# Optimization experiments

Measured on AMD Instinct MI355X. Metric: run time of the kernel, lower is better.

The kernel has to match this reference:

```python
import jax, jax.numpy as jnp
import numpy as np
import math

H, KVH, DH = 8, 1, 256
CAP = 50.0
THETA = 10000.0
HIDDEN = [2048, 1024, 1024]


def _rope_cos_sin(pos, dh=DH, theta=THETA):
    # pos: [b, s] int -> cos/sin: [b, s, dh] (Gemma style: freqs duplicated)
    inv_freq = 1.0 / (theta ** (jnp.arange(0, dh, 2, dtype=jnp.float32) / dh))
    freqs = pos.astype(jnp.float32)[..., None] * inv_freq  # [b, s, dh/2]
    emb = jnp.concatenate([freqs, freqs], axis=-1)
    return jnp.cos(emb), jnp.sin(emb)


def _rotate_half(x):
    x1, x2 = jnp.split(x, 2, axis=-1)
    return jnp.concatenate([-x2, x1], axis=-1)


def _apply_rope(q, k, cos, sin):
    # q: [b,H,s,d], k: [b,KVH,s,d]; cos/sin: [b,s,d] -> broadcast over heads
    c = cos[:, None].astype(q.dtype)
    s = sin[:, None].astype(q.dtype)
    return q * c + _rotate_half(q) * s, k * c + _rotate_half(k) * s


def setup_inputs() -> dict:
    key = jax.random.key(0)
    ks = jax.random.split(key, 32)
    inp = {
        'hs0': jax.random.normal(ks[0], (8, 968, 2048), jnp.float32),
        'hs1': jax.random.normal(ks[1], (8, 6, 1024), jnp.float32),
        'hs2': jax.random.normal(ks[2], (8, 50, 1024), jnp.float32),
        'attention_mask': jnp.zeros((8, 1, 1024, 1024), jnp.float32),
        'pos0': jnp.sort(jax.random.randint(ks[3], (8, 968), 0, 1024), axis=-1),
        'pos1': jnp.sort(jax.random.randint(ks[4], (8, 6), 0, 1024), axis=-1),
        'pos2': jnp.sort(jax.random.randint(ks[5], (8, 50), 0, 1024), axis=-1),
    }
    ki = 6
    for b, hid in enumerate(HIDDEN):
        inp[f'wq{b}'] = 0.02 * jax.random.normal(ks[ki + 0], (hid, H * DH), jnp.float32)
        inp[f'wk{b}'] = 0.02 * jax.random.normal(ks[ki + 1], (hid, KVH * DH), jnp.float32)
        inp[f'wv{b}'] = 0.02 * jax.random.normal(ks[ki + 2], (hid, KVH * DH), jnp.float32)
        inp[f'wo{b}'] = 0.02 * jax.random.normal(ks[ki + 3], (H * DH, hid), jnp.float32)
        ki += 4
    return inp


def _joint_attn(hs_all, pos_all, mask, wq, wk, wv, wo):
    b = hs_all[0].shape[0]
    q_lens = [h.shape[1] for h in hs_all]
    qs, kss, vs = [], [], []
    for hs, pos, Wq, Wk, Wv in zip(hs_all, pos_all, wq, wk, wv):
        s = hs.shape[1]
        q = (hs @ Wq).reshape(b, s, H, DH).transpose(0, 2, 1, 3)
        k = (hs @ Wk).reshape(b, s, KVH, DH).transpose(0, 2, 1, 3)
        v = (hs @ Wv).reshape(b, s, KVH, DH).transpose(0, 2, 1, 3)
        cos, sin = _rope_cos_sin(pos)
        q, k = _apply_rope(q, k, cos, sin)
        # repeat_kv: MQA -> expand KV heads to H
        qs.append(q)
        kss.append(jnp.repeat(k, H // KVH, axis=1))
        vs.append(jnp.repeat(v, H // KVH, axis=1))
    q = jnp.concatenate(qs, axis=2)   # [b,H,S,d]
    k = jnp.concatenate(kss, axis=2)
    v = jnp.concatenate(vs, axis=2)
    scores = jnp.einsum('bhqd,bhkd->bhqk', q, k) / math.sqrt(DH)
    scores = jnp.tanh(scores / CAP) * CAP + mask  # tanh soft-capping
    p = jax.nn.softmax(scores.astype(jnp.float32), axis=-1).astype(q.dtype)
    out = jnp.einsum('bhqk,bhkd->bhqd', p, v)     # [b,H,S,d]
    out = out.transpose(0, 2, 1, 3).reshape(b, sum(q_lens), H * DH)
    outs, off = [], 0
    for ql, Wo in zip(q_lens, wo):
        outs.append(out[:, off:off + ql] @ Wo)
        off += ql
    return tuple(outs)


def reference(hs0, hs1, hs2, attention_mask, pos0, pos1, pos2,
              wq0, wk0, wv0, wo0, wq1, wk1, wv1, wo1, wq2, wk2, wv2, wo2):
    return _joint_attn((hs0, hs1, hs2), (pos0, pos1, pos2), attention_mask,
                       (wq0, wq1, wq2), (wk0, wk1, wk2), (wv0, wv1, wv2),
                       (wo0, wo1, wo2))
```

## Files before the change

### kernel.cpp

```cpp
#include <hip/hip_runtime.h>
#include <hip/hip_bf16.h>
#include <math.h>

namespace {
constexpr int Bn = 8, Sn = 1024, Hn = 8, DHn = 256, HDn = 2048;
constexpr size_t QB0 = 0;
constexpr size_t QB1 = (size_t)20 * 64 * 4096;
constexpr size_t QB2 = QB1 + (size_t)20 * 32 * 4096;
constexpr size_t HB0 = 0;
constexpr size_t HB1 = (size_t)61 * 64 * 4096;
constexpr size_t HB2 = HB1 + (size_t)1 * 32 * 4096;
constexpr size_t OB0 = 0;
constexpr size_t OB1 = (size_t)16 * 64 * 4096;
constexpr size_t OB2 = OB1 + (size_t)8 * 64 * 4096;
}

using bf16x8 = __attribute__((ext_vector_type(8))) short;
using f32x4  = __attribute__((ext_vector_type(4))) float;
using i32x4  = __attribute__((ext_vector_type(4))) int;

__device__ __forceinline__ float bf2f(unsigned short u) {
  unsigned int x = ((unsigned int)u) << 16;
  return __builtin_bit_cast(float, x);
}
__device__ __forceinline__ unsigned short f2bf(float f) {
  unsigned int x = __builtin_bit_cast(unsigned int, f);
  x += 0x7fff + ((x >> 16) & 1);
  return (unsigned short)(x >> 16);
}
__device__ __forceinline__ bf16x8 pack8(const float4& u, const float4& v) {
  bf16x8 r;
  r[0] = (short)f2bf(u.x); r[1] = (short)f2bf(u.y); r[2] = (short)f2bf(u.z); r[3] = (short)f2bf(u.w);
  r[4] = (short)f2bf(v.x); r[5] = (short)f2bf(v.y); r[6] = (short)f2bf(v.z); r[7] = (short)f2bf(v.w);
  return r;
}
__device__ __forceinline__ void gload_lds16(const void* g, void* l) {
  __builtin_amdgcn_global_load_lds(
      (const __attribute__((address_space(1))) void*)g,
      (__attribute__((address_space(3))) void*)l, 16, 0, 0);
}
__device__ __forceinline__ unsigned cvtpk(float lo, float hi) {
  unsigned r;
  asm("v_cvt_pk_bf16_f32 %0, %1, %2" : "=v"(r) : "v"(lo), "v"(hi));
  return r;
}

__device__ __forceinline__ void convW_body(
    const float* __restrict__ W, unsigned short* __restrict__ dstBase,
    int K, int N, int nb, int kb, float (*S)[132], int t)
{
  const int kl = t >> 5, nq = (t & 31) * 4;
  for (int kk = kl; kk < 64; kk += 8) {
    const float4 v = *(const float4*)(W + (size_t)(kb * 64 + kk) * N + nb * 128 + nq);
    S[kk][nq] = v.x; S[kk][nq + 1] = v.y; S[kk][nq + 2] = v.z; S[kk][nq + 3] = v.w;
  }
  __syncthreads();
  unsigned short* chunk = dstBase + ((size_t)nb * (K >> 5) + kb * 2) * 4096;
#pragma unroll
  for (int j = 0; j < 4; ++j) {
    const int q = t * 4 + j;
    const int r = q >> 3, g = q & 7;
    bf16x8 o;
#pragma unroll
    for (int e = 0; e < 8; ++e) o[e] = (short)f2bf(S[g * 8 + e][r]);
    *(bf16x8*)(chunk + (g >> 2) * 4096 + r * 32 + (((g & 3) ^ ((r >> 1) & 3)) * 8)) = o;
  }
}

__global__ __launch_bounds__(256) void convAll(
    const float* __restrict__ wq0, const float* __restrict__ wk0, const float* __restrict__ wv0,
    const float* __restrict__ wq1, const float* __restrict__ wk1, const float* __restrict__ wv1,
    const float* __restrict__ wq2, const float* __restrict__ wk2, const float* __restrict__ wv2,
    const float* __restrict__ hs0, const float* __restrict__ hs1, const float* __restrict__ hs2,
    unsigned short* __restrict__ qkvT, unsigned short* __restrict__ hsT)
{
  __shared__ float S[64][132];
  const int bid = blockIdx.x;
  const int t = threadIdx.x;

  if (bid < 1280) {
    const float* W; unsigned short* dst; int K, N, nb, kb;
    if (bid < 512)       { W = wq0; dst = qkvT + QB0;                  K = 2048; N = 2048; nb = bid & 15; kb = bid >> 4; }
    else if (bid < 576)  { int r = bid - 512;  W = wk0; dst = qkvT + QB0 + (size_t)16 * 64 * 4096; K = 2048; N = 256; nb = r & 1; kb = r >> 1; }
    else if (bid < 640)  { int r = bid - 576;  W = wv0; dst = qkvT + QB0 + (size_t)18 * 64 * 4096; K = 2048; N = 256; nb = r & 1; kb = r >> 1; }
    else if (bid < 896)  { int r = bid - 640;  W = wq1; dst = qkvT + QB1;                  K = 1024; N = 2048; nb = r & 15; kb = r >> 4; }
    else if (bid < 928)  { int r = bid - 896;  W = wk1; dst = qkvT + QB1 + (size_t)16 * 32 * 4096; K = 1024; N = 256; nb = r & 1; kb = r >> 1; }
    else if (bid < 960)  { int r = bid - 928;  W = wv1; dst = qkvT + QB1 + (size_t)18 * 32 * 4096; K = 1024; N = 256; nb = r & 1; kb = r >> 1; }
    else if (bid < 1216) { int r = bid - 960;  W = wq2; dst = qkvT + QB2;                  K = 1024; N = 2048; nb = r & 15; kb = r >> 4; }
    else if (bid < 1248) { int r = bid - 1216; W = wk2; dst = qkvT + QB2 + (size_t)16 * 32 * 4096; K = 1024; N = 256; nb = r & 1; kb = r >> 1; }
    else                 { int r = bid - 1248; W = wv2; dst = qkvT + QB2 + (size_t)18 * 32 * 4096; K = 1024; N = 256; nb = r & 1; kb = r >> 1; }
    convW_body(W, dst, K, N, nb, kb, S, t);
  } else {
    const float* A; unsigned short* dst; int K, M_total, mb, kb;
    if (bid < 3232)      { int it = bid - 1280; A = hs0; dst = hsT + HB0; K = 2048; M_total = 7744; mb = it >> 5; kb = it & 31; }
    else if (bid < 3248) { int it = bid - 3232; A = hs1; dst = hsT + HB1; K = 1024; M_total = 48;   mb = 0;       kb = it; }
    else                 { int it = bid - 3248; A = hs2; dst = hsT + HB2; K = 1024; M_total = 400;  mb = it >> 4; kb = it & 15; }
    unsigned short* chunk = dst + ((size_t)mb * (K >> 5) + kb * 2) * 4096;
#pragma unroll
    for (int j = 0; j < 4; ++j) {
      const int q = j * 256 + t;
      const int r = q >> 3, g = q & 7;
      int m = mb * 128 + r;
      if (m >= M_total) m = mb * 128;
      const float* src = A + (size_t)m * K + kb * 64 + g * 8;
      const float4 u = *(const float4*)(src);
      const float4 v = *(const float4*)(src + 4);
      *(bf16x8*)(chunk + (g >> 2) * 4096 + r * 32 + (((g & 3) ^ ((r >> 1) & 3)) * 8)) = pack8(u, v);
    }
  }
}

__global__ __launch_bounds__(256) void convWo(
    const float* __restrict__ wo0, const float* __restrict__ wo1, const float* __restrict__ wo2,
    unsigned short* __restrict__ woT)
{
  __shared__ float S[64][132];
  const int bid = blockIdx.x;
  const float* W; unsigned short* dst; int N, nb, kb;
  if (bid < 512)      { W = wo0; dst = woT + OB0; N = 2048; nb = bid & 15; kb = bid >> 4; }
  else if (bid < 768) { int r = bid - 512; W = wo1; dst = woT + OB1; N = 1024; nb = r & 7; kb = r >> 3; }
  else                { int r = bid - 768; W = wo2; dst = woT + OB2; N = 1024; nb = r & 7; kb = r >> 3; }
  convW_body(W, dst, HDn, N, nb, kb, S, threadIdx.x);
}

__global__ __launch_bounds__(256) void gemm_qkv(
    const unsigned short* __restrict__ hsT, const unsigned short* __restrict__ qkvT,
    unsigned short* __restrict__ Qh, unsigned short* __restrict__ Kh,
    unsigned short* __restrict__ Vt)
{
  __shared__ __align__(16) short As[2][4096];
  __shared__ __align__(16) short Bs[2][4096];
  const int tid = threadIdx.x;
  const int w  = tid >> 6, l = tid & 63;
  const int wm = w >> 1,  wn = w & 1;
  const int lc = l & 15,  lg = l >> 4;

  const int bid = blockIdx.x;
  int bx, by, L, K, c_off, M_total;
  const unsigned short *aBase, *wBase;
  if (bid < 1220)      { bx = bid % 20; by = bid / 20; L = 968; K = 2048; c_off = 0;   M_total = 7744; aBase = hsT + HB0; wBase = qkvT + QB0; }
  else if (bid < 1240) { bx = bid - 1220; by = 0;      L = 6;   K = 1024; c_off = 968; M_total = 48;   aBase = hsT + HB1; wBase = qkvT + QB1; }
  else                 { int r = bid - 1240; bx = r % 20; by = r / 20; L = 50; K = 1024; c_off = 974; M_total = 400; aBase = hsT + HB2; wBase = qkvT + QB2; }
  const int kcN = K >> 5;
  const int bm0 = by * 128;

  int region, nbL, cb0;
  if (bx < 16)      { region = 0; nbL = bx;      cb0 = bx * 128; }
  else if (bx < 18) { region = 1; nbL = bx - 16; cb0 = (bx - 16) * 128; }
  else              { region = 2; nbL = bx - 18; cb0 = (bx - 18) * 128; }
  const unsigned short* WTr = wBase +
      (region == 0 ? (size_t)0 : (region == 1 ? (size_t)16 * kcN * 4096
                                              : (size_t)18 * kcN * 4096));
  const char* bChunk0 = (const char*)(WTr + (size_t)nbL * kcN * 4096);
  const char* aChunk0 = (const char*)(aBase + (size_t)by * kcN * 4096);

  f32x4 acc[4][4];
#pragma unroll
  for (int i = 0; i < 4; ++i)
#pragma unroll
    for (int j = 0; j < 4; ++j) acc[i][j] = (f32x4){0.f, 0.f, 0.f, 0.f};

  auto issue = [&](int kc, int nb) {
    const char* sa = aChunk0 + (size_t)kc * 8192;
    const char* sb = bChunk0 + (size_t)kc * 8192;
    char* da = (char*)&As[nb][0];
    char* db = (char*)&Bs[nb][0];
    gload_lds16(sa + tid * 16, da + tid * 16);
    gload_lds16(sa + tid * 16 + 4096, da + tid * 16 + 4096);
    gload_lds16(sb + tid * 16, db + tid * 16);
    gload_lds16(sb + tid * 16 + 4096, db + tid * 16 + 4096);
  };

  issue(0, 0);
  for (int kt = 0; kt < kcN; ++kt) {
    const int cur = kt & 1;
    __builtin_amdgcn_s_barrier();
    if (kt + 1 < kcN) {
      issue(kt + 1, cur ^ 1);
      asm volatile("s_waitcnt vmcnt(4)" ::: "memory");
    } else {
      asm volatile("s_waitcnt vmcnt(0)" ::: "memory");
    }
    __builtin_amdgcn_s_barrier();
    __builtin_amdgcn_sched_barrier(0);
    bf16x8 af[4], bfg[4];
#pragma unroll
    for (int mi = 0; mi < 4; ++mi) {
      const int row = wm * 64 + mi * 16 + lc;
      af[mi] = *(const bf16x8*)((const char*)&As[cur][0] + row * 64 +
                                ((lg ^ ((row >> 1) & 3)) * 16));
    }
#pragma unroll
    for (int ni = 0; ni < 4; ++ni) {
      const int row = wn * 64 + ni * 16 + lc;
      bfg[ni] = *(const bf16x8*)((const char*)&Bs[cur][0] + row * 64 +
                                 ((lg ^ ((row >> 1) & 3)) * 16));
    }
#pragma unroll
    for (int mi = 0; mi < 4; ++mi)
#pragma unroll
      for (int ni = 0; ni < 4; ++ni)
        acc[mi][ni] = __builtin_amdgcn_mfma_f32_16x16x32_bf16(af[mi], bfg[ni], acc[mi][ni], 0, 0, 0);
  }

#pragma unroll
  for (int mi = 0; mi < 4; ++mi) {
    const int gm = bm0 + wm * 64 + mi * 16 + lg * 4;
#pragma unroll
    for (int r = 0; r < 4; ++r) {
      const int m = gm + r;
      if (m < M_total) {
        const int cb = m / L, cs = m - cb * L;
#pragma unroll
        for (int ni = 0; ni < 4; ++ni) {
          const int colL = cb0 + wn * 64 + ni * 16 + lc;
          const unsigned short v = f2bf(acc[mi][ni][r]);
          if (region == 0) {
            const int hh = colL >> 8, dd = colL & 255;
            Qh[(((size_t)cb * Hn + hh) * Sn + c_off + cs) * DHn + dd] = v;
          } else if (region == 1) {
            Kh[((size_t)cb * Sn + c_off + cs) * DHn + colL] = v;
          } else {
            Vt[((size_t)cb * DHn + colL) * Sn + c_off + cs] = v;
          }
        }
      }
    }
  }
}

__global__ __launch_bounds__(256) void gemm_wo(
    const unsigned short* __restrict__ A, const unsigned short* __restrict__ woT,
    float* __restrict__ C)
{
  __shared__ __align__(16) short As[2][4096];
  __shared__ __align__(16) short Bs[2][4096];
  const int tid = threadIdx.x;
  const int w  = tid >> 6, l = tid & 63;
  const int wm = w >> 1,  wn = w & 1;
  const int lc = l & 15,  lg = l >> 4;

  const int bid = blockIdx.x;
  int bx, by, L, N, a_off, M_total;
  const unsigned short* wb;
  float* Cg;
  if (bid < 976)      { bx = bid & 15; by = bid >> 4; L = 968; N = 2048; a_off = 0;   M_total = 7744; wb = woT + OB0; Cg = C; }
  else if (bid < 984) { bx = bid - 976; by = 0;       L = 6;   N = 1024; a_off = 968; M_total = 48;   wb = woT + OB1; Cg = C + (size_t)7744 * 2048; }
  else                { int r = bid - 984; bx = r & 7; by = r >> 3; L = 50; N = 1024; a_off = 974; M_total = 400; wb = woT + OB2; Cg = C + (size_t)7744 * 2048 + (size_t)48 * 1024; }
  const int bm0 = by * 128;
  const char* chunk0 = (const char*)(wb + (size_t)bx * 64 * 4096);

  const int gcont = (tid & 3) ^ ((tid >> 3) & 3);
  const char* aRow[2];
#pragma unroll
  for (int j = 0; j < 2; ++j) {
    int m = bm0 + (tid >> 2) + j * 64;
    if (m >= M_total) m = 0;
    const int cb = m / L, cs = m - cb * L;
    aRow[j] = (const char*)(A + (size_t)(cb * Sn + a_off + cs) * HDn) + gcont * 16;
  }

  f32x4 acc[4][4];
#pragma unroll
  for (int i = 0; i < 4; ++i)
#pragma unroll
    for (int j = 0; j < 4; ++j) acc[i][j] = (f32x4){0.f, 0.f, 0.f, 0.f};

  auto issue = [&](int kc, int nb) {
    char* da = (char*)&As[nb][0];
    char* db = (char*)&Bs[nb][0];
    gload_lds16(aRow[0] + (size_t)kc * 64, da + tid * 16);
    gload_lds16(aRow[1] + (size_t)kc * 64, da + tid * 16 + 4096);
    const char* sb = chunk0 + (size_t)kc * 8192;
    gload_lds16(sb + tid * 16, db + tid * 16);
    gload_lds16(sb + tid * 16 + 4096, db + tid * 16 + 4096);
  };

  issue(0, 0);
  for (int kt = 0; kt < 64; ++kt) {
    const int cur = kt & 1;
    __builtin_amdgcn_s_barrier();
    if (kt + 1 < 64) {
      issue(kt + 1, cur ^ 1);
      asm volatile("s_waitcnt vmcnt(4)" ::: "memory");
    } else {
      asm volatile("s_waitcnt vmcnt(0)" ::: "memory");
    }
    __builtin_amdgcn_s_barrier();
    __builtin_amdgcn_sched_barrier(0);
    bf16x8 af[4], bfg[4];
#pragma unroll
    for (int mi = 0; mi < 4; ++mi) {
      const int row = wm * 64 + mi * 16 + lc;
      af[mi] = *(const bf16x8*)((const char*)&As[cur][0] + row * 64 +
                                ((lg ^ ((row >> 1) & 3)) * 16));
    }
#pragma unroll
    for (int ni = 0; ni < 4; ++ni) {
      const int row = wn * 64 + ni * 16 + lc;
      bfg[ni] = *(const bf16x8*)((const char*)&Bs[cur][0] + row * 64 +
                                 ((lg ^ ((row >> 1) & 3)) * 16));
    }
#pragma unroll
    for (int mi = 0; mi < 4; ++mi)
#pragma unroll
      for (int ni = 0; ni < 4; ++ni)
        acc[mi][ni] = __builtin_amdgcn_mfma_f32_16x16x32_bf16(af[mi], bfg[ni], acc[mi][ni], 0, 0, 0);
  }

#pragma unroll
  for (int mi = 0; mi < 4; ++mi) {
    const int gm = bm0 + wm * 64 + mi * 16 + lg * 4;
#pragma unroll
    for (int r = 0; r < 4; ++r) {
      const int m = gm + r;
      if (m < M_total) {
        const int cb = m / L, cs = m - cb * L;
#pragma unroll
        for (int ni = 0; ni < 4; ++ni) {
          const int col = bx * 128 + wn * 64 + ni * 16 + lc;
          Cg[(size_t)(cb * L + cs) * N + col] = acc[mi][ni][r];
        }
      }
    }
  }
}

__global__ __launch_bounds__(128) void rope_k(
    unsigned short* __restrict__ Kh,
    const int* __restrict__ p0, const int* __restrict__ p1, const int* __restrict__ p2)
{
  const int t = blockIdx.x, b = t >> 10, s = t & 1023;
  int p;
  if (s < 968)      p = p0[b * 968 + s];
  else if (s < 974) p = p1[b * 6 + (s - 968)];
  else              p = p2[b * 50 + (s - 974)];
  const float pf = (float)p;
  const float c0 = -0.07195578415606394f;
  const int d = threadIdx.x;
  const float inv = __expf(c0 * (float)d);
  float cs, sn;
  sincosf(pf * inv, &sn, &cs);
  unsigned short* base = Kh + ((size_t)b * Sn + s) * DHn;
  const float x1 = bf2f(base[d]), x2 = bf2f(base[d + 128]);
  base[d]       = f2bf(x1 * cs - x2 * sn);
  base[d + 128] = f2bf(x2 * cs + x1 * sn);
}

__global__ __launch_bounds__(512) void attn_mfma(
    const unsigned short* __restrict__ Qh, const unsigned short* __restrict__ Kh,
    const unsigned short* __restrict__ Vt, const float* __restrict__ mask,
    const int* __restrict__ p0, const int* __restrict__ p1, const int* __restrict__ p2,
    unsigned short* __restrict__ O)
{
  __shared__ __align__(16) short KsB[2][8192];
  __shared__ __align__(16) short VsB[2][8192];
  __shared__ __align__(16) float Ms[2][512];
  const int tid = threadIdx.x;
  const int w  = tid >> 6;
  const int l  = tid & 63;
  const int lc = l & 15;
  const int lg = l >> 4;
  const int bid = blockIdx.x;
  const int b  = bid & 7;
  const int q0 = (bid >> 3) * 16;
  const int srow = q0 + lc;

  const char* KgB = (const char*)(Kh + (size_t)b * Sn * DHn);
  const char* VgB = (const char*)(Vt + (size_t)b * DHn * Sn);

  auto stage = [&](int kt, int nb) {
    const char* kg = KgB + (size_t)kt * 16384;
    const char* vg = VgB + (size_t)kt * 64;
#pragma unroll
    for (int j = 0; j < 2; ++j) {
      const int chunk = w * 2 + j;
      const int o = chunk * 1024 + l * 16;
      const int srcK = o ^ (((o >> 9) & 7) << 4);
      gload_lds16(kg + srcK, (char*)&KsB[nb][0] + chunk * 1024);
    }
#pragma unroll
    for (int j = 0; j < 2; ++j) {
      const int chunk = w * 2 + j;
      const int o = chunk * 1024 + l * 16;
      const int x = o ^ (((o >> 7) & 3) << 4);
      gload_lds16(vg + (size_t)(x >> 6) * 2048 + (x & 63),
                  (char*)&VsB[nb][0] + chunk * 1024);
    }
    if (l < 16) {
      const int q = 2 * w + (l >> 3);
      const int kb = (((l & 7) * 4) - 4 * q) & 31;
      const float* mg = mask + ((size_t)b * Sn + q0 + q) * Sn + kt * 32 + kb;
      gload_lds16(mg, (char*)&Ms[nb][0] + w * 256);
    }
  };

  stage(0, 0);

  int p;
  if (srow < 968)      p = p0[b * 968 + srow];
  else if (srow < 974) p = p1[b * 6 + (srow - 968)];
  else                 p = p2[b * 50 + (srow - 974)];
  const float pf = (float)p;
  const float c0 = -0.07195578415606394f;

  const unsigned short* qrow = Qh + (((size_t)b * Hn + w) * Sn + srow) * DHn;
  bf16x8 qf[8];
#pragma unroll
  for (int dt = 0; dt < 8; ++dt)
    qf[dt] = *(const bf16x8*)(qrow + dt * 32 + lg * 8);
#pragma unroll
  for (int dt = 0; dt < 4; ++dt) {
#pragma unroll
    for (int j = 0; j < 8; ++j) {
      const int d = dt * 32 + lg * 8 + j;
      const float inv = __expf(c0 * (float)d);
      float cs, sn;
      sincosf(pf * inv, &sn, &cs);
      const float x1 = bf2f((unsigned short)qf[dt][j]);
      const float x2 = bf2f((unsigned short)qf[dt + 4][j]);
      qf[dt][j]     = (short)f2bf(x1 * cs - x2 * sn);
      qf[dt + 4][j] = (short)f2bf(x2 * cs + x1 * sn);
    }
  }

  f32x4 accO[16];
#pragma unroll
  for (int i = 0; i < 16; ++i) accO[i] = (f32x4){0.f, 0.f, 0.f, 0.f};
  float lsum = 0.f;

  const float C1 = 3.6067376022e-3f;
  const float RC = -144.26950408889634f;
  const float L2E = 1.4426950408889634f;

  const int mo0 = lc * 128 + (((lg * 4) + 4 * lc) & 31) * 4;
  const int mo1 = lc * 128 + (((16 + lg * 4) + 4 * lc) & 31) * 4;
  const int sidx0 = (((lg & 1) * 2) * 16 + lc) * 4;
  const int sidx1 = sidx0 + 64;
  const bool hiT = (lg >= 2);

  int cur = 0;
  for (int kt = 0; kt < 32; ++kt) {
    if (kt + 1 < 32) {
      stage(kt + 1, cur ^ 1);
      asm volatile("s_waitcnt vmcnt(5)" ::: "memory");
    } else {
      asm volatile("s_waitcnt vmcnt(0)" ::: "memory");
    }
    __builtin_amdgcn_s_barrier();
    __builtin_amdgcn_sched_barrier(0);

    const char* Ks = (const char*)&KsB[cur][0];
    const char* Vs = (const char*)&VsB[cur][0];
    const char* Mw = (const char*)&Ms[cur][0];

    const float4 mv0 = *(const float4*)(Mw + mo0);
    const float4 mv1 = *(const float4*)(Mw + mo1);

    f32x4 sc[2];
    __builtin_amdgcn_s_setprio(1);
#pragma unroll
    for (int ct = 0; ct < 2; ++ct) {
      f32x4 a0 = (f32x4){0.f, 0.f, 0.f, 0.f};
      f32x4 a1 = (f32x4){0.f, 0.f, 0.f, 0.f};
      const int row = ct * 16 + lc;
      const int sw = (row & 7) << 4;
#pragma unroll
      for (int dt = 0; dt < 8; dt += 2) {
        const int byt0 = (row * 512 + dt * 64 + lg * 16) ^ sw;
        const int byt1 = (row * 512 + (dt + 1) * 64 + lg * 16) ^ sw;
        const bf16x8 kf0 = *(const bf16x8*)(Ks + byt0);
        const bf16x8 kf1 = *(const bf16x8*)(Ks + byt1);
        a0 = __builtin_amdgcn_mfma_f32_16x16x32_bf16(kf0, qf[dt], a0, 0, 0, 0);
        a1 = __builtin_amdgcn_mfma_f32_16x16x32_bf16(kf1, qf[dt + 1], a1, 0, 0, 0);
      }
      sc[ct] = a0 + a1;
    }
    __builtin_amdgcn_s_setprio(0);

    const float mA[8] = {mv0.x, mv0.y, mv0.z, mv0.w, mv1.x, mv1.y, mv1.z, mv1.w};
    float pr[8];
#pragma unroll
    for (int t = 0; t < 2; ++t) {
#pragma unroll
      for (int r = 0; r < 4; ++r) {
        const float e2 = __builtin_amdgcn_exp2f(sc[t][r] * C1);
        const float rr = __builtin_amdgcn_rcpf(e2 + 1.f);
        const float pv = __builtin_amdgcn_exp2f(fmaf(rr, RC, mA[t * 4 + r] * L2E));
        lsum += pv;
        pr[t * 4 + r] = pv;
      }
    }

    const int t0w0 = (int)cvtpk(pr[0], pr[1]);
    const int t0w1 = (int)cvtpk(pr[2], pr[3]);
    const int t1w0 = (int)cvtpk(pr[4], pr[5]);
    const int t1w1 = (int)cvtpk(pr[6], pr[7]);
    const int b00 = __builtin_amdgcn_ds_bpermute(sidx0, t0w0);
    const int b01 = __builtin_amdgcn_ds_bpermute(sidx0, t0w1);
    const int b02 = __builtin_amdgcn_ds_bpermute(sidx1, t0w0);
    const int b03 = __builtin_amdgcn_ds_bpermute(sidx1, t0w1);
    const int b10 = __builtin_amdgcn_ds_bpermute(sidx0, t1w0);
    const int b11 = __builtin_amdgcn_ds_bpermute(sidx0, t1w1);
    const int b12 = __builtin_amdgcn_ds_bpermute(sidx1, t1w0);
    const int b13 = __builtin_amdgcn_ds_bpermute(sidx1, t1w1);
    i32x4 pd;
    pd[0] = hiT ? b10 : b00;
    pd[1] = hiT ? b11 : b01;
    pd[2] = hiT ? b12 : b02;
    pd[3] = hiT ? b13 : b03;
    const bf16x8 pfr = __builtin_bit_cast(bf16x8, pd);

    __builtin_amdgcn_s_setprio(1);
#pragma unroll
    for (int nt = 0; nt < 16; ++nt) {
      const int row = nt * 16 + lc;
      const int byt = (row * 64 + lg * 16) ^ (((row >> 1) & 3) << 4);
      const bf16x8 vf = *(const bf16x8*)(Vs + byt);
      accO[nt] = __builtin_amdgcn_mfma_f32_16x16x32_bf16(pfr, vf, accO[nt], 0, 0, 0);
    }
    __builtin_amdgcn_s_setprio(0);

    __builtin_amdgcn_s_barrier();
    cur ^= 1;
  }

  lsum += __shfl_xor(lsum, 16);
  lsum += __shfl_xor(lsum, 32);
  const float rinvF = 1.f / lsum;
  float rv[4];
#pragma unroll
  for (int r = 0; r < 4; ++r) rv[r] = __shfl(rinvF, lg * 4 + r);

  unsigned short* obase = O + ((size_t)b * Sn + q0 + lg * 4) * HDn + w * DHn + lc;
#pragma unroll
  for (int nt = 0; nt < 16; ++nt)
#pragma unroll
    for (int r = 0; r < 4; ++r)
      obase[(size_t)r * HDn + nt * 16] = f2bf(accO[nt][r] * rv[r]);
}

extern "C" void kernel_launch(void* const* d_in, const int* in_sizes, int n_in,
                              void* d_out, int out_size, void* d_ws, size_t ws_size,
                              hipStream_t stream) {
  (void)in_sizes; (void)n_in; (void)out_size; (void)ws_size;
  const float* hs0  = (const float*)d_in[0];
  const float* hs1  = (const float*)d_in[1];
  const float* hs2  = (const float*)d_in[2];
  const float* mask = (const float*)d_in[3];
  const int*   pos0 = (const int*)d_in[4];
  const int*   pos1 = (const int*)d_in[5];
  const int*   pos2 = (const int*)d_in[6];
  float* out = (float*)d_out;

  unsigned short* Qh = (unsigned short*)d_ws;
  unsigned short* Kh = Qh + (size_t)Bn * Sn * HDn;
  unsigned short* Vt = Kh + (size_t)Bn * Sn * DHn;
  unsigned short* Ob = Vt + (size_t)Bn * Sn * DHn;
  unsigned short* qkvT = Ob;
  unsigned short* woT  = Qh;
  unsigned short* hsT  = (unsigned short*)out;

  hipLaunchKernelGGL(convAll, dim3(3312), dim3(256), 0, stream,
                     (const float*)d_in[7],  (const float*)d_in[8],  (const float*)d_in[9],
                     (const float*)d_in[11], (const float*)d_in[12], (const float*)d_in[13],
                     (const float*)d_in[15], (const float*)d_in[16], (const float*)d_in[17],
                     hs0, hs1, hs2, qkvT, hsT);

  hipLaunchKernelGGL(gemm_qkv, dim3(1320), dim3(256), 0, stream,
                     hsT, qkvT, Qh, Kh, Vt);

  hipLaunchKernelGGL(rope_k, dim3(Bn * Sn), dim3(128), 0, stream, Kh, pos0, pos1, pos2);
  hipLaunchKernelGGL(attn_mfma, dim3(512), dim3(512), 0, stream,
                     Qh, Kh, Vt, mask, pos0, pos1, pos2, Ob);

  hipLaunchKernelGGL(convWo, dim3(1024), dim3(256), 0, stream,
                     (const float*)d_in[10], (const float*)d_in[14], (const float*)d_in[18], woT);

  hipLaunchKernelGGL(gemm_wo, dim3(1016), dim3(256), 0, stream, Ob, woT, out);
}
```

Baseline: 425.3 us.

## Enlarge Wo GEMM tiles to 256x256 with 512 threads and interleaved prefetch

Rewrites the output-projection GEMM to use 256x256 block tiles with 8 waves, each computing 128x64, and a 128KB LDS double buffer staging two K-steps per stage. Global-to-LDS loads for the next stage are interleaved with the MFMA sub-blocks, and MFMA sections run at raised wave priority. The aim is higher arithmetic intensity per loaded byte and fewer barriers per K-step. In exchange, occupancy drops to one block per CU, and the grid shrinks to 260 blocks, which may underfill the GPU and waste work on the small segments.

```diff
diff --git a/kernel.cpp b/kernel.cpp
--- a/kernel.cpp
+++ b/kernel.cpp
@@ -229,88 +229,93 @@
   }
 }
 
-__global__ __launch_bounds__(256) void gemm_wo(
+__global__ __launch_bounds__(512) void gemm_wo(
     const unsigned short* __restrict__ A, const unsigned short* __restrict__ woT,
     float* __restrict__ C)
 {
-  __shared__ __align__(16) short As[2][4096];
-  __shared__ __align__(16) short Bs[2][4096];
+  __shared__ __align__(16) char lds[131072];
   const int tid = threadIdx.x;
   const int w  = tid >> 6, l = tid & 63;
-  const int wm = w >> 1,  wn = w & 1;
+  const int wm = w >> 2,  wn = w & 3;
   const int lc = l & 15,  lg = l >> 4;
 
   const int bid = blockIdx.x;
-  int bx, by, L, N, a_off, M_total;
+  int u, t, L, N, a_off, M_total;
   const unsigned short* wb;
   float* Cg;
-  if (bid < 976)      { bx = bid & 15; by = bid >> 4; L = 968; N = 2048; a_off = 0;   M_total = 7744; wb = woT + OB0; Cg = C; }
-  else if (bid < 984) { bx = bid - 976; by = 0;       L = 6;   N = 1024; a_off = 968; M_total = 48;   wb = woT + OB1; Cg = C + (size_t)7744 * 2048; }
-  else                { int r = bid - 984; bx = r & 7; by = r >> 3; L = 50; N = 1024; a_off = 974; M_total = 400; wb = woT + OB2; Cg = C + (size_t)7744 * 2048 + (size_t)48 * 1024; }
-  const int bm0 = by * 128;
-  const char* chunk0 = (const char*)(wb + (size_t)bx * 64 * 4096);
+  if (bid < 248)      { u = bid & 7; t = bid >> 3; L = 968; N = 2048; a_off = 0;   M_total = 7744; wb = woT + OB0; Cg = C; }
+  else if (bid < 252) { u = bid - 248; t = 0;      L = 6;   N = 1024; a_off = 968; M_total = 48;   wb = woT + OB1; Cg = C + (size_t)7744 * 2048; }
+  else                { int r = bid - 252; u = r & 3; t = r >> 2; L = 50; N = 1024; a_off = 974; M_total = 400; wb = woT + OB2; Cg = C + (size_t)7744 * 2048 + (size_t)48 * 1024; }
 
   const int gcont = (tid & 3) ^ ((tid >> 3) & 3);
-  const char* aRow[2];
-#pragma unroll
-  for (int j = 0; j < 2; ++j) {
-    int m = bm0 + (tid >> 2) + j * 64;
+  const char* aP[2];
+#pragma unroll
+  for (int rh = 0; rh < 2; ++rh) {
+    int m = t * 256 + rh * 128 + (tid >> 2);
     if (m >= M_total) m = 0;
     const int cb = m / L, cs = m - cb * L;
-    aRow[j] = (const char*)(A + (size_t)(cb * Sn + a_off + cs) * HDn) + gcont * 16;
-  }
-
-  f32x4 acc[4][4];
-#pragma unroll
-  for (int i = 0; i < 4; ++i)
+    aP[rh] = (const char*)(A + (size_t)(cb * Sn + a_off + cs) * HDn) + gcont * 16;
+  }
+  const char* bP[2];
+  bP[0] = (const char*)(wb + (size_t)(2 * u) * 64 * 4096);
+  bP[1] = (const char*)(wb + (size_t)(2 * u + 1) * 64 * 4096);
+
+  auto stage_chunk = [&](int st, int ci, int buf) {
+    char* dst = lds + buf * 65536 + ci * 8192 + tid * 16;
+    const int kh = ci >> 2;
+    const size_t kidx = (size_t)(2 * st + kh);
+    if ((ci & 2) == 0) gload_lds16(aP[ci & 1] + kidx * 64, dst);
+    else               gload_lds16(bP[ci & 1] + kidx * 8192 + tid * 16, dst);
+  };
+
+  f32x4 acc[8][4];
+#pragma unroll
+  for (int i = 0; i < 8; ++i)
 #pragma unroll
     for (int j = 0; j < 4; ++j) acc[i][j] = (f32x4){0.f, 0.f, 0.f, 0.f};
 
-  auto issue = [&](int kc, int nb) {
-    char* da = (char*)&As[nb][0];
-    char* db = (char*)&Bs[nb][0];
-    gload_lds16(aRow[0] + (size_t)kc * 64, da + tid * 16);
-    gload_lds16(aRow[1] + (size_t)kc * 64, da + tid * 16 + 4096);
-    const char* sb = chunk0 + (size_t)kc * 8192;
-    gload_lds16(sb + tid * 16, db + tid * 16);
-    gload_lds16(sb + tid * 16 + 4096, db + tid * 16 + 4096);
-  };
-
-  issue(0, 0);
-  for (int kt = 0; kt < 64; ++kt) {
-    const int cur = kt & 1;
-    __builtin_amdgcn_s_barrier();
-    if (kt + 1 < 64) {
-      issue(kt + 1, cur ^ 1);
-      asm volatile("s_waitcnt vmcnt(4)" ::: "memory");
-    } else {
-      asm volatile("s_waitcnt vmcnt(0)" ::: "memory");
-    }
-    __builtin_amdgcn_s_barrier();
-    __builtin_amdgcn_sched_barrier(0);
-    bf16x8 af[4], bfg[4];
-#pragma unroll
-    for (int mi = 0; mi < 4; ++mi) {
-      const int row = wm * 64 + mi * 16 + lc;
-      af[mi] = *(const bf16x8*)((const char*)&As[cur][0] + row * 64 +
-                                ((lg ^ ((row >> 1) & 3)) * 16));
-    }
-#pragma unroll
-    for (int ni = 0; ni < 4; ++ni) {
-      const int row = wn * 64 + ni * 16 + lc;
-      bfg[ni] = *(const bf16x8*)((const char*)&Bs[cur][0] + row * 64 +
-                                 ((lg ^ ((row >> 1) & 3)) * 16));
-    }
-#pragma unroll
-    for (int mi = 0; mi < 4; ++mi)
+  const int gk16 = (lg ^ ((lc >> 1) & 3)) * 16;
+  const int aRowB = lc * 64 + gk16;
+  const int bRowB = ((wn & 1) * 64 + lc) * 64 + gk16;
+
+#pragma unroll
+  for (int ci = 0; ci < 8; ++ci) stage_chunk(0, ci, 0);
+
+  for (int s = 0; s < 32; ++s) {
+    const int cur = s & 1;
+    const char* rb = lds + cur * 65536;
+#pragma unroll
+    for (int kk = 0; kk < 2; ++kk) {
+      if (s == 31 && kk == 1) { asm volatile("s_waitcnt vmcnt(0)" ::: "memory"); }
+      else                    { asm volatile("s_waitcnt vmcnt(4)" ::: "memory"); }
+      __builtin_amdgcn_s_barrier();
+
+      const char* aC = rb + (kk * 4 + wm) * 8192;
+      const char* bC = rb + (kk * 4 + 2 + (wn >> 1)) * 8192;
+      bf16x8 bfg[4];
 #pragma unroll
       for (int ni = 0; ni < 4; ++ni)
-        acc[mi][ni] = __builtin_amdgcn_mfma_f32_16x16x32_bf16(af[mi], bfg[ni], acc[mi][ni], 0, 0, 0);
-  }
-
-#pragma unroll
-  for (int mi = 0; mi < 4; ++mi) {
-    const int gm = bm0 + wm * 64 + mi * 16 + lg * 4;
+        bfg[ni] = *(const bf16x8*)(bC + bRowB + ni * 1024);
+
+#pragma unroll
+      for (int sub = 0; sub < 4; ++sub) {
+        if (s < 31) stage_chunk(s + 1, kk * 4 + sub, cur ^ 1);
+        const bf16x8 af0 = *(const bf16x8*)(aC + aRowB + (2 * sub) * 1024);
+        const bf16x8 af1 = *(const bf16x8*)(aC + aRowB + (2 * sub + 1) * 1024);
+        __builtin_amdgcn_s_setprio(1);
+#pragma unroll
+        for (int ni = 0; ni < 4; ++ni) {
+          acc[2 * sub][ni]     = __builtin_amdgcn_mfma_f32_16x16x32_bf16(af0, bfg[ni], acc[2 * sub][ni], 0, 0, 0);
+          acc[2 * sub + 1][ni] = __builtin_amdgcn_mfma_f32_16x16x32_bf16(af1, bfg[ni], acc[2 * sub + 1][ni], 0, 0, 0);
+        }
+        __builtin_amdgcn_s_setprio(0);
+      }
+    }
+  }
+
+#pragma unroll
+  for (int mi = 0; mi < 8; ++mi) {
+    const int gm = t * 256 + wm * 128 + mi * 16 + lg * 4;
 #pragma unroll
     for (int r = 0; r < 4; ++r) {
       const int m = gm + r;
@@ -318,7 +323,7 @@
         const int cb = m / L, cs = m - cb * L;
 #pragma unroll
         for (int ni = 0; ni < 4; ++ni) {
-          const int col = bx * 128 + wn * 64 + ni * 16 + lc;
+          const int col = u * 256 + wn * 64 + ni * 16 + lc;
           Cg[(size_t)(cb * L + cs) * N + col] = acc[mi][ni][r];
         }
       }
@@ -577,5 +582,5 @@
   hipLaunchKernelGGL(convWo, dim3(1024), dim3(256), 0, stream,
                      (const float*)d_in[10], (const float*)d_in[14], (const float*)d_in[18], woT);
 
-  hipLaunchKernelGGL(gemm_wo, dim3(1016), dim3(256), 0, stream, Ob, woT, out);
-}
+  hipLaunchKernelGGL(gemm_wo, dim3(260), dim3(512), 0, stream, Ob, woT, out);
+}
```

After: 437.7 us. +2.9%, slower.
